# Kernel optimization log

Hardware: AMD Instinct MI355X
Metric: run time of the kernel (lower is better)

The kernel has to match this reference:

```python
import jax, jax.numpy as jnp
import numpy as np
from jax import lax

SEQ_LENGTH = 32
B, I, O = 1024, 2048, 1024
DT = 1e-3
TAU_PRE, TAU_POST = 0.02, 0.02
ETA_PLUS, ETA_MINUS = 1e-3, 1e-3
W_MIN, W_MAX = -1.0, 1.0
TAU_MEM = 0.02
V_TH = 1.0


def setup_inputs() -> dict:
    key = jax.random.key(0)
    k1, k2, k3 = jax.random.split(key, 3)
    # Bernoulli(0.05) input spikes, rate-coded, reused each timestep
    input_spikes = (jax.random.uniform(k1, (B, I)) < 0.05).astype(jnp.float32)
    weight = jax.random.normal(k2, (O, I), dtype=jnp.float32) * (1.0 / np.sqrt(I))
    bias = jax.random.normal(k3, (O,), dtype=jnp.float32) * 0.01
    return {"input_spikes": input_spikes, "weight": weight, "bias": bias}


def reference(input_spikes, weight, bias):
    decay_pre = jnp.exp(jnp.float32(-DT / TAU_PRE))
    decay_post = jnp.exp(jnp.float32(-DT / TAU_POST))
    v_decay = jnp.exp(jnp.float32(-DT / TAU_MEM))

    b = input_spikes.shape[0]
    v0 = jnp.zeros((b, O), dtype=input_spikes.dtype)
    z0 = jnp.zeros((b, O), dtype=input_spikes.dtype)
    # STDPState(t_pre=1.0, t_post=1.0) broadcast to trace shapes
    tpre0 = jnp.ones((b, I), dtype=input_spikes.dtype)
    tpost0 = jnp.ones((b, O), dtype=input_spikes.dtype)

    def step(carry, _):
        v, w, tpre, tpost, _z = carry
        # linear projection with current (plastic) weights
        z_in = input_spikes @ w.T + bias  # [B, O]
        # LIF output neuron: decay, integrate, threshold, reset
        v = v * v_decay + z_in
        z_out = (v >= V_TH).astype(v.dtype)
        v = v * (1.0 - z_out)
        # STDP trace update: decay then accumulate spikes
        tpre = tpre * decay_pre + input_spikes
        tpost = tpost * decay_post + z_out
        # spike-gated eligibility outer products, summed over batch
        dw = (ETA_PLUS * jnp.einsum('bo,bi->oi', z_out, tpre)
              - ETA_MINUS * jnp.einsum('bo,bi->oi', tpost, input_spikes))
        w = jnp.clip(w + dw, W_MIN, W_MAX)
        return (v, w, tpre, tpost, z_out), None

    (v, w, tpre, tpost, z_out), _ = lax.scan(
        step, (v0, weight, tpre0, tpost0, z0), None, length=SEQ_LENGTH)
    return z_out, v, w
```

## Files before the change

### kernel.cpp

```cpp
#include <hip/hip_runtime.h>
#include <cmath>

#define SEQ 32
#define BB 1024
#define II 2048
#define OO 1024

typedef unsigned short ushortt;

__global__ void build_idx_rev(const float* __restrict__ x, ushortt* __restrict__ idxArr,
                              int* __restrict__ cntArr, int* __restrict__ rcnt,
                              ushortt* __restrict__ rev, ushortt* __restrict__ idxT) {
  int b = blockIdx.x;
  int lane = threadIdx.x;
  __shared__ ushortt sIdx[256];
  const float* row = x + (long)b * II;
  int base = 0;
  for (int c = 0; c < II / 64; ++c) {
    float val = row[c * 64 + lane];
    unsigned long long m = __ballot(val != 0.0f);
    if (val != 0.0f) {
      int pos = base + __popcll(m & ((1ull << lane) - 1ull));
      if (pos < 256) {
        idxArr[(b << 8) + pos] = (ushortt)(c * 64 + lane);
        sIdx[pos] = (ushortt)(c * 64 + lane);
      }
    }
    base += __popcll(m);
  }
  int cnt = base < 256 ? base : 256;
  if (lane == 0) cntArr[b] = cnt;
  __syncthreads();
  {
    int j0 = lane * 4;
    ushort4 u;
    u.x = (j0 + 0 < cnt) ? sIdx[j0 + 0] : (ushortt)II;
    u.y = (j0 + 1 < cnt) ? sIdx[j0 + 1] : (ushortt)II;
    u.z = (j0 + 2 < cnt) ? sIdx[j0 + 2] : (ushortt)II;
    u.w = (j0 + 3 < cnt) ? sIdx[j0 + 3] : (ushortt)II;
    ((ushort4*)idxT)[(lane << 10) + b] = u;
  }
  for (int j = lane; j < cnt; j += 64) {
    int i = sIdx[j];
    int pos = atomicAdd(&rcnt[i], 1);
    if (pos < 128) rev[((long)i << 7) + pos] = (ushortt)b;
  }
}

__global__ void transpose2_f32(const float* __restrict__ zC, const float* __restrict__ vC,
                               float* __restrict__ oz, float* __restrict__ ov) {
  __shared__ float t[32][33];
  const float* src = blockIdx.z ? vC : zC;
  float* dst = blockIdx.z ? ov : oz;
  int c0 = blockIdx.x * 32, r0 = blockIdx.y * 32;
  int tx = threadIdx.x, ty = threadIdx.y;
#pragma unroll
  for (int k = 0; k < 4; k++)
    t[ty + k * 8][tx] = src[(long)(r0 + ty + k * 8) * BB + c0 + tx];
  __syncthreads();
#pragma unroll
  for (int k = 0; k < 4; k++)
    dst[(long)(c0 + ty + k * 8) * OO + r0 + tx] = t[tx][ty + k * 8];
}

__global__ __launch_bounds__(512, 8) void snn_kernel(
    const float* __restrict__ w, const float* __restrict__ bias,
    const ushortt* __restrict__ idxT, const int* __restrict__ cntArr,
    const int* __restrict__ rcnt, const ushortt* __restrict__ rev,
    const ushortt* __restrict__ idxArr,
    float* __restrict__ zC, float* __restrict__ vC, float* __restrict__ outw,
    float dec) {
  int o = blockIdx.x, tid = threadIdx.x, lane = tid & 63, wave = tid >> 6;
  __shared__ float2 wa[II + 1];
  __shared__ float mLb[II + 1];
  __shared__ int sList[BB];
  __shared__ float SnuD[BB];
  __shared__ int sCnt, sFlag, cFlag;
  float* mL = mLb;
  float* nT = mLb;
  float* Sfix = mLb;
  float* SAD = (float*)sList;

  float n4[4];
#pragma unroll
  for (int q = 0; q < 4; ++q) {
    int i = q * 512 + tid;
    float nv = (float)rcnt[i];
    wa[i] = make_float2(w[(long)o * II + i], 0.f);
    nT[i] = nv;
    n4[q] = nv;
  }
#pragma unroll
  for (int k = 0; k < 2; ++k) SnuD[k * 512 + tid] = 0.f;
  int cb[2];
#pragma unroll
  for (int k = 0; k < 2; ++k) cb[k] = cntArr[k * 512 + tid];
  if (tid == 0) {
    sFlag = 0; cFlag = 0;
    wa[II] = make_float2(0.f, 0.f);
    nT[II] = 0.f;
  }

  float bo = bias[o];
  unsigned clipped = 0;
  bool everSpk = false;
  float p = 1.f, u = 1.f;
  __syncthreads();

  const ushort4* tpb = (const ushort4*)idxT;
  double S[2];
  float Snu[2], SA[2], v4[2], zk[2];
#pragma unroll
  for (int k = 0; k < 2; ++k) {
    int b = k * 512 + tid;
    double s0 = 0.0, s1 = 0.0;
    float sn0 = 0.f, sn1 = 0.f;
    int jm4 = (cb[k] + 3) >> 2;
    const ushort4* tp = tpb + b;
    for (int g = 0; g < jm4; ++g) {
      ushort4 u0 = tp[(g << 10)];
      s0 += (double)wa[u0.x].x; sn0 += nT[u0.x];
      s1 += (double)wa[u0.y].x; sn1 += nT[u0.y];
      s0 += (double)wa[u0.z].x; sn0 += nT[u0.z];
      s1 += (double)wa[u0.w].x; sn1 += nT[u0.w];
    }
    S[k] = s0 + s1; Snu[k] = sn0 + sn1;
    SA[k] = 0.f; v4[k] = 0.f; zk[k] = 0.f;
  }
  __syncthreads();
#pragma unroll
  for (int k = 0; k < 2; ++k) {
    int b = k * 512 + tid;
    Sfix[b] = 0.f; SAD[b] = 0.f;
  }

  for (int t = 0; t < SEQ; ++t) {
    p *= dec; u *= dec; u += 1.f;
    float spre = u - p;
    int local = 0;
#pragma unroll
    for (int k = 0; k < 2; ++k) {
      float zin = (float)S[k] + bo;
      float nv = v4[k] * dec + zin;
      float z = (nv >= 1.f) ? 1.f : 0.f;
      nv = nv * (1.f - z);
      v4[k] = nv; zk[k] = z;
      if (z != 0.f) local = 1;
    }
    if (local) sFlag = 1;
    __syncthreads();
    int spk = sFlag;

    if (!spk) {
#pragma unroll
      for (int q = 0; q < 4; ++q) {
        int i = q * 512 + tid;
        bool already = (clipped >> q) & 1u;
        float n = 0.f, atn = 0.f, fix = 0.f;
        bool cl = false;
        if (!already) {
          float2 tq = wa[i];
          n = n4[q];
          atn = everSpk ? (dec * tq.y) : 0.f;
          float dw = -(1e-3f * (p * n + atn));
          float pre = tq.x + dw;
          float wv = fminf(fmaxf(pre, -1.f), 1.f);
          cl = (pre <= -1.f);
          if (cl) {
            clipped |= 1u << q;
            fix = (-1.f - tq.x) - dw;
            wa[i] = make_float2(wv, 0.f);
          } else {
            wa[i] = make_float2(wv, atn);
          }
        }
        unsigned long long m = __ballot(cl);
        if (m) {
          if (lane == 0) cFlag = 1;
          while (m) {
            int src = __builtin_ctzll(m);
            m &= m - 1;
            int ii = __shfl(i, src);
            float fx = __shfl(fix, src);
            float mn = -__shfl(n, src);
            float ma = -__shfl(atn, src);
            int rc = rcnt[ii];
            const ushortt* rp = rev + ((long)ii << 7);
            for (int r = lane; r < rc; r += 64) {
              int b2 = rp[r];
              atomicAdd(&Sfix[b2], fx);
              atomicAdd(&SnuD[b2], mn);
              if (everSpk) atomicAdd(&SAD[b2], ma);
            }
          }
        }
      }
      __syncthreads();
      float coefP = 1e-3f * p;
      if (cFlag) {
#pragma unroll
        for (int k = 0; k < 2; ++k) {
          int b = k * 512 + tid;
          S[k] = S[k] - (double)coefP * (double)Snu[k]
                      - (double)1e-3f * (double)(dec * SA[k])
                      + (double)Sfix[b];
          SA[k] = dec * SA[k] + SAD[b];
          Snu[k] = Snu[k] + SnuD[b];
          Sfix[b] = 0.f; SnuD[b] = 0.f; SAD[b] = 0.f;
        }
      } else {
#pragma unroll
        for (int k = 0; k < 2; ++k) {
          S[k] = S[k] - (double)coefP * (double)Snu[k]
                      - (double)1e-3f * (double)(dec * SA[k]);
          SA[k] = dec * SA[k];
        }
      }
      if (tid == 0) { sFlag = 0; cFlag = 0; }
      __syncthreads();
    } else {
      everSpk = true;
      if (tid == 0) sCnt = 0;
      __syncthreads();
#pragma unroll
      for (int k = 0; k < 2; ++k)
        if (zk[k] != 0.f) { int pos = atomicAdd(&sCnt, 1); sList[pos] = k * 512 + tid; }
#pragma unroll
      for (int q = 0; q < 4; ++q) mL[q * 512 + tid] = 0.f;
      __syncthreads();
      int ns = sCnt;
      for (int s = wave; s < ns; s += 8) {
        int b = sList[s];
        int cbb = cntArr[b];
        const ushortt* ip = idxArr + (b << 8);
        for (int j = lane; j < cbb; j += 64)
          atomicAdd(&mL[ip[j]], 1.f);
      }
      __syncthreads();
      float cv = (float)ns;
#pragma unroll
      for (int q = 0; q < 4; ++q) {
        int i = q * 512 + tid;
        float2 tq = wa[i];
        float mt = mL[i];
        float atn = dec * tq.y + mt;
        float n = n4[q];
        float dw = 1e-3f * (p * cv + spre * mt) - 1e-3f * (p * n + atn);
        float pre = tq.x + dw;
        float wv = fminf(fmaxf(pre, -1.f), 1.f);
        bool cl = (pre <= -1.f);
        bool was = (clipped >> q) & 1u;
        if (cl) clipped |= 1u << q; else clipped &= ~(1u << q);
        wa[i] = make_float2(wv, cl ? 0.f : atn);
        bool flip = (cl != was);
        float dn = cl ? -n : n;
        unsigned long long m = __ballot(flip);
        while (m) {
          int src = __builtin_ctzll(m);
          m &= m - 1;
          int ii = __shfl(i, src);
          float d = __shfl(dn, src);
          int rc = rcnt[ii];
          const ushortt* rp = rev + ((long)ii << 7);
          for (int r = lane; r < rc; r += 64)
            atomicAdd(&SnuD[rp[r]], d);
        }
      }
      __syncthreads();
#pragma unroll
      for (int k = 0; k < 2; ++k) {
        int b = k * 512 + tid;
        double s0 = 0.0, s1 = 0.0;
        float sa0 = 0.f, sa1 = 0.f;
        int jm4 = (cb[k] + 3) >> 2;
        const ushort4* tp = tpb + b;
        for (int g = 0; g < jm4; ++g) {
          ushort4 u0 = tp[(g << 10)];
          float2 e0 = wa[u0.x], e1 = wa[u0.y], e2 = wa[u0.z], e3 = wa[u0.w];
          s0 += (double)e0.x; sa0 += e0.y;
          s1 += (double)e1.x; sa1 += e1.y;
          s0 += (double)e2.x; sa0 += e2.y;
          s1 += (double)e3.x; sa1 += e3.y;
        }
        S[k] = s0 + s1; SA[k] = sa0 + sa1;
        Snu[k] = Snu[k] + SnuD[b];
        SnuD[b] = 0.f;
        Sfix[b] = 0.f; SAD[b] = 0.f;
      }
      if (tid == 0) { sFlag = 0; cFlag = 0; }
      __syncthreads();
    }
  }

  __syncthreads();
#pragma unroll
  for (int q = 0; q < 4; ++q) outw[(long)o * II + q * 512 + tid] = wa[q * 512 + tid].x;
#pragma unroll
  for (int k = 0; k < 2; ++k) {
    int b = k * 512 + tid;
    zC[(long)o * BB + b] = zk[k];
    vC[(long)o * BB + b] = v4[k];
  }
}

extern "C" void kernel_launch(void* const* d_in, const int* in_sizes, int n_in,
                              void* d_out, int out_size, void* d_ws, size_t ws_size,
                              hipStream_t stream) {
  const float* x = (const float*)d_in[0];
  const float* w = (const float*)d_in[1];
  const float* bias = (const float*)d_in[2];
  float* out = (float*)d_out;

  char* ws = (char*)d_ws;
  ushortt* idxArr = (ushortt*)(ws + 0);
  int* cntArr = (int*)(ws + 524288);
  ushortt* idxT = (ushortt*)(ws + 528384);
  int* rcnt = (int*)(ws + 1060864);
  ushortt* rev = (ushortt*)(ws + 1069056);
  float* zC = (float*)(ws + 1593344);
  float* vC = (float*)(ws + 5787648);

  hipMemsetAsync(rcnt, 0, II * sizeof(int), stream);
  build_idx_rev<<<BB, 64, 0, stream>>>(x, idxArr, cntArr, rcnt, rev, idxT);

  const float dec = (float)exp(-0.05);

  snn_kernel<<<OO, 512, 0, stream>>>(w, bias, idxT, cntArr, rcnt, rev, idxArr,
                                     zC, vC, out + 2 * BB * OO, dec);

  transpose2_f32<<<dim3(BB / 32, OO / 32, 2), dim3(32, 8), 0, stream>>>(zC, vC, out, out + BB * OO);
}
```

Baseline: 283.8 us.

## Vectorize index build, use wave-uniform loop bounds, trim register state

The index-building kernel now reads four floats per lane with float4 loads and four ballots instead of one float per iteration. In the main kernel, per-thread trip counts for the gather loops become the wave-wide maximum count, so loop control is uniform (padded entries point at a zero sentinel). The n4 and cb register arrays are dropped, with rcnt re-read from global memory in the update loops, and the dual double accumulators are merged into one. This lowers register pressure and divergence at the cost of extra global loads, padded gather iterations, and a longer serial double-add chain.

Measured after the change: 280.2 us. Within noise of the previous version (-1.3%).

```diff
diff --git a/kernel.cpp b/kernel.cpp
--- a/kernel.cpp
+++ b/kernel.cpp
@@ -14,19 +14,24 @@
   int b = blockIdx.x;
   int lane = threadIdx.x;
   __shared__ ushortt sIdx[256];
-  const float* row = x + (long)b * II;
+  const float4* row4 = (const float4*)(x + (long)b * II);
   int base = 0;
-  for (int c = 0; c < II / 64; ++c) {
-    float val = row[c * 64 + lane];
-    unsigned long long m = __ballot(val != 0.0f);
-    if (val != 0.0f) {
-      int pos = base + __popcll(m & ((1ull << lane) - 1ull));
-      if (pos < 256) {
-        idxArr[(b << 8) + pos] = (ushortt)(c * 64 + lane);
-        sIdx[pos] = (ushortt)(c * 64 + lane);
-      }
-    }
-    base += __popcll(m);
+  for (int c4 = 0; c4 < II / 256; ++c4) {
+    float4 v = row4[c4 * 64 + lane];
+    unsigned long long m0 = __ballot(v.x != 0.f);
+    unsigned long long m1 = __ballot(v.y != 0.f);
+    unsigned long long m2 = __ballot(v.z != 0.f);
+    unsigned long long m3 = __ballot(v.w != 0.f);
+    unsigned long long below = (1ull << lane) - 1ull;
+    int pre = __popcll(m0 & below) + __popcll(m1 & below) +
+              __popcll(m2 & below) + __popcll(m3 & below);
+    int col0 = c4 * 256 + lane * 4;
+    int pos = base + pre;
+    if (v.x != 0.f) { if (pos < 256) { idxArr[(b << 8) + pos] = (ushortt)col0;       sIdx[pos] = (ushortt)col0; }       ++pos; }
+    if (v.y != 0.f) { if (pos < 256) { idxArr[(b << 8) + pos] = (ushortt)(col0 + 1); sIdx[pos] = (ushortt)(col0 + 1); } ++pos; }
+    if (v.z != 0.f) { if (pos < 256) { idxArr[(b << 8) + pos] = (ushortt)(col0 + 2); sIdx[pos] = (ushortt)(col0 + 2); } ++pos; }
+    if (v.w != 0.f) { if (pos < 256) { idxArr[(b << 8) + pos] = (ushortt)(col0 + 3); sIdx[pos] = (ushortt)(col0 + 3); } ++pos; }
+    base += __popcll(m0) + __popcll(m1) + __popcll(m2) + __popcll(m3);
   }
   int cnt = base < 256 ? base : 256;
   if (lane == 0) cntArr[b] = cnt;
@@ -81,26 +86,28 @@
   float* Sfix = mLb;
   float* SAD = (float*)sList;
 
-  float n4[4];
 #pragma unroll
   for (int q = 0; q < 4; ++q) {
     int i = q * 512 + tid;
-    float nv = (float)rcnt[i];
     wa[i] = make_float2(w[(long)o * II + i], 0.f);
-    nT[i] = nv;
-    n4[q] = nv;
+    nT[i] = (float)rcnt[i];
   }
 #pragma unroll
   for (int k = 0; k < 2; ++k) SnuD[k * 512 + tid] = 0.f;
-  int cb[2];
-#pragma unroll
-  for (int k = 0; k < 2; ++k) cb[k] = cntArr[k * 512 + tid];
   if (tid == 0) {
     sFlag = 0; cFlag = 0;
     wa[II] = make_float2(0.f, 0.f);
     nT[II] = 0.f;
   }
 
+  int jmax[2];
+#pragma unroll
+  for (int k = 0; k < 2; ++k) {
+    int c = cntArr[k * 512 + wave * 64 + lane];
+#pragma unroll
+    for (int off = 32; off > 0; off >>= 1) c = max(c, __shfl_xor(c, off));
+    jmax[k] = c;
+  }
   float bo = bias[o];
   unsigned clipped = 0;
   bool everSpk = false;
@@ -113,18 +120,18 @@
 #pragma unroll
   for (int k = 0; k < 2; ++k) {
     int b = k * 512 + tid;
-    double s0 = 0.0, s1 = 0.0;
-    float sn0 = 0.f, sn1 = 0.f;
-    int jm4 = (cb[k] + 3) >> 2;
+    double s = 0.0;
+    float sn = 0.f;
+    int jm4 = (jmax[k] + 3) >> 2;
     const ushort4* tp = tpb + b;
     for (int g = 0; g < jm4; ++g) {
       ushort4 u0 = tp[(g << 10)];
-      s0 += (double)wa[u0.x].x; sn0 += nT[u0.x];
-      s1 += (double)wa[u0.y].x; sn1 += nT[u0.y];
-      s0 += (double)wa[u0.z].x; sn0 += nT[u0.z];
-      s1 += (double)wa[u0.w].x; sn1 += nT[u0.w];
+      s += (double)wa[u0.x].x; sn += nT[u0.x];
+      s += (double)wa[u0.y].x; sn += nT[u0.y];
+      s += (double)wa[u0.z].x; sn += nT[u0.z];
+      s += (double)wa[u0.w].x; sn += nT[u0.w];
     }
-    S[k] = s0 + s1; Snu[k] = sn0 + sn1;
+    S[k] = s; Snu[k] = sn;
     SA[k] = 0.f; v4[k] = 0.f; zk[k] = 0.f;
   }
   __syncthreads();
@@ -160,7 +167,7 @@
         bool cl = false;
         if (!already) {
           float2 tq = wa[i];
-          n = n4[q];
+          n = (float)rcnt[i];
           atn = everSpk ? (dec * tq.y) : 0.f;
           float dw = -(1e-3f * (p * n + atn));
           float pre = tq.x + dw;
@@ -244,7 +251,7 @@
         float2 tq = wa[i];
         float mt = mL[i];
         float atn = dec * tq.y + mt;
-        float n = n4[q];
+        float n = (float)rcnt[i];
         float dw = 1e-3f * (p * cv + spre * mt) - 1e-3f * (p * n + atn);
         float pre = tq.x + dw;
         float wv = fminf(fmaxf(pre, -1.f), 1.f);
@@ -270,19 +277,19 @@
 #pragma unroll
       for (int k = 0; k < 2; ++k) {
         int b = k * 512 + tid;
-        double s0 = 0.0, s1 = 0.0;
-        float sa0 = 0.f, sa1 = 0.f;
-        int jm4 = (cb[k] + 3) >> 2;
+        double s = 0.0;
+        float sa = 0.f;
+        int jm4 = (jmax[k] + 3) >> 2;
         const ushort4* tp = tpb + b;
         for (int g = 0; g < jm4; ++g) {
           ushort4 u0 = tp[(g << 10)];
           float2 e0 = wa[u0.x], e1 = wa[u0.y], e2 = wa[u0.z], e3 = wa[u0.w];
-          s0 += (double)e0.x; sa0 += e0.y;
-          s1 += (double)e1.x; sa1 += e1.y;
-          s0 += (double)e2.x; sa0 += e2.y;
-          s1 += (double)e3.x; sa1 += e3.y;
-        }
-        S[k] = s0 + s1; SA[k] = sa0 + sa1;
+          s += (double)e0.x; sa += e0.y;
+          s += (double)e1.x; sa += e1.y;
+          s += (double)e2.x; sa += e2.y;
+          s += (double)e3.x; sa += e3.y;
+        }
+        S[k] = s; SA[k] = sa;
         Snu[k] = Snu[k] + SnuD[b];
         SnuD[b] = 0.f;
         Sfix[b] = 0.f; SAD[b] = 0.f;
```
